# Kernel tuning notes

Measured on AMD Instinct MI355X. Metric: run time of the kernel, lower is better.

The kernel has to match this reference:

```python
import jax, jax.numpy as jnp
import numpy as np

GRID = (32, 32, 32)  # (W, H, D) from init_kwargs gridshape


def setup_inputs() -> dict:
    key = jax.random.key(0)
    k1, k2 = jax.random.split(key)
    N, F = 500000, 128
    features = jax.random.normal(k1, (N, F), dtype=jnp.float32)
    points = jax.random.uniform(k2, (N, 3), dtype=jnp.float32)  # locations in [0,1)^3
    return {"features": features, "points": points}


def reference(features, points):
    W, H, D = GRID
    # voxel index per point: floor(p * [W,H,D]), clipped into the grid
    dims = jnp.array([W, H, D], dtype=points.dtype)
    idx = jnp.floor(points * dims).astype(jnp.int32)
    idx = jnp.clip(idx, 0, jnp.array([W - 1, H - 1, D - 1], dtype=jnp.int32))
    cell = idx[:, 0] * (H * D) + idx[:, 1] * D + idx[:, 2]  # flat cell id [N]
    # scatter-max of point features into cells
    pooled = jax.ops.segment_max(features, cell, num_segments=W * H * D)
    # CUDA kernel initializes feat_cells to 0 (indices -1): empty cells and
    # cells whose max feature is negative stay at 0.
    return jnp.maximum(pooled, 0.0)
```

## Files before the change

### kernel.cpp

```cpp
#include <hip/hip_runtime.h>


constexpr int NCELL = 32 * 32 * 32;
constexpr int CAP   = 64;
constexpr int NF    = 128;

__global__ void bin_kernel(const float* __restrict__ points,
                           int* __restrict__ count,
                           int* __restrict__ bins, int n) {
    int i = blockIdx.x * blockDim.x + threadIdx.x;
    if (i >= n) return;
    float x = points[3 * i + 0] * 32.0f;
    float y = points[3 * i + 1] * 32.0f;
    float z = points[3 * i + 2] * 32.0f;
    int ix = (int)floorf(x); ix = ix < 0 ? 0 : (ix > 31 ? 31 : ix);
    int iy = (int)floorf(y); iy = iy < 0 ? 0 : (iy > 31 ? 31 : iy);
    int iz = (int)floorf(z); iz = iz < 0 ? 0 : (iz > 31 ? 31 : iz);
    int cell = (ix << 10) | (iy << 5) | iz;
    int slot = atomicAdd(&count[cell], 1);
    if (slot < CAP) bins[(cell << 6) + slot] = i;
}

__global__ __launch_bounds__(NF) void reduce_kernel(
        const float* __restrict__ feats,
        const int* __restrict__ count,
        const int* __restrict__ bins,
        float* __restrict__ out) {
    int cell = blockIdx.x;
    int t = threadIdx.x;
    int cnt = count[cell];
    if (cnt > CAP) cnt = CAP;
    const int* bp = bins + (cell << 6);

    float m = 0.0f;
    int k = 0;
    for (; k + 4 <= cnt; k += 4) {
        int p0 = bp[k], p1 = bp[k + 1], p2 = bp[k + 2], p3 = bp[k + 3];
        float a = feats[(size_t)p0 * NF + t];
        float b = feats[(size_t)p1 * NF + t];
        float c = feats[(size_t)p2 * NF + t];
        float d = feats[(size_t)p3 * NF + t];
        m = fmaxf(m, fmaxf(fmaxf(a, b), fmaxf(c, d)));
    }
    for (; k < cnt; k++)
        m = fmaxf(m, feats[(size_t)bp[k] * NF + t]);

    out[((size_t)cell << 7) + t] = m;
}

extern "C" void kernel_launch(void* const* d_in, const int* in_sizes, int n_in,
                              void* d_out, int out_size, void* d_ws, size_t ws_size,
                              hipStream_t stream) {
    const float* features = (const float*)d_in[0];
    const float* points   = (const float*)d_in[1];
    int n = in_sizes[1] / 3;

    int* bins  = (int*)d_ws;
    int* count = (int*)((char*)d_ws + (size_t)NCELL * CAP * 4);

    hipMemsetAsync(count, 0, NCELL * sizeof(int), stream);

    bin_kernel<<<(n + 255) / 256, 256, 0, stream>>>(points, count, bins, n);

    reduce_kernel<<<NCELL, NF, 0, stream>>>(
        features, count, bins, (float*)d_out);
}
```

Before: 383.9 us.

## Split cell reduction across four point groups with float4 loads

The reduce kernel now assigns 32 lanes per point, each loading a float4, so one block handles four points at once instead of walking them one after another. Bin indices are staged in shared memory, and the four partial maxima are combined through shared memory before a single float4 store. This gives more memory parallelism per block and wider loads, at the cost of two barriers and a final reduction step done by only 32 threads.

```diff
diff --git a/kernel.cpp b/kernel.cpp
--- a/kernel.cpp
+++ b/kernel.cpp
@@ -21,31 +21,50 @@
     if (slot < CAP) bins[(cell << 6) + slot] = i;
 }
 
-__global__ __launch_bounds__(NF) void reduce_kernel(
-        const float* __restrict__ feats,
+__device__ __forceinline__ float4 max4(float4 a, float4 b) {
+    float4 r;
+    r.x = fmaxf(a.x, b.x); r.y = fmaxf(a.y, b.y);
+    r.z = fmaxf(a.z, b.z); r.w = fmaxf(a.w, b.w);
+    return r;
+}
+
+__global__ __launch_bounds__(128) void reduce_kernel(
+        const float4* __restrict__ feats4,
         const int* __restrict__ count,
         const int* __restrict__ bins,
-        float* __restrict__ out) {
+        float4* __restrict__ out4) {
     int cell = blockIdx.x;
-    int t = threadIdx.x;
+    int tid  = threadIdx.x;
+    int lane = tid & 31;
+    int g    = tid >> 5;
+
+    __shared__ int    sbins[CAP];
+    __shared__ float4 part[4][32];
+
     int cnt = count[cell];
     if (cnt > CAP) cnt = CAP;
-    const int* bp = bins + (cell << 6);
+    if (tid < CAP) sbins[tid] = bins[(cell << 6) + tid];
+    __syncthreads();
 
-    float m = 0.0f;
-    int k = 0;
-    for (; k + 4 <= cnt; k += 4) {
-        int p0 = bp[k], p1 = bp[k + 1], p2 = bp[k + 2], p3 = bp[k + 3];
-        float a = feats[(size_t)p0 * NF + t];
-        float b = feats[(size_t)p1 * NF + t];
-        float c = feats[(size_t)p2 * NF + t];
-        float d = feats[(size_t)p3 * NF + t];
-        m = fmaxf(m, fmaxf(fmaxf(a, b), fmaxf(c, d)));
+    float4 m = make_float4(0.f, 0.f, 0.f, 0.f);
+    int k = g;
+    for (; k + 4 < cnt; k += 8) {
+        int p0 = sbins[k], p1 = sbins[k + 4];
+        float4 a = feats4[(size_t)p0 * 32 + lane];
+        float4 b = feats4[(size_t)p1 * 32 + lane];
+        m = max4(m, max4(a, b));
     }
-    for (; k < cnt; k++)
-        m = fmaxf(m, feats[(size_t)bp[k] * NF + t]);
+    if (k < cnt)
+        m = max4(m, feats4[(size_t)sbins[k] * 32 + lane]);
 
-    out[((size_t)cell << 7) + t] = m;
+    part[g][lane] = m;
+    __syncthreads();
+
+    if (tid < 32) {
+        float4 a = part[0][tid], b = part[1][tid];
+        float4 c = part[2][tid], d = part[3][tid];
+        out4[(size_t)cell * 32 + tid] = max4(max4(a, b), max4(c, d));
+    }
 }
 
 extern "C" void kernel_launch(void* const* d_in, const int* in_sizes, int n_in,
@@ -62,6 +81,6 @@
 
     bin_kernel<<<(n + 255) / 256, 256, 0, stream>>>(points, count, bins, n);
 
-    reduce_kernel<<<NCELL, NF, 0, stream>>>(
-        features, count, bins, (float*)d_out);
+    reduce_kernel<<<NCELL, 128, 0, stream>>>(
+        (const float4*)features, count, bins, (float4*)d_out);
 }
```

Result: no change. 382.2 us (-0.4%).

## Vectorize reduce kernel with float4 loads and one wave per cell

Applied to the files above, without the earlier changes.

Rewrites the reduce kernel so each 64-lane wave handles one cell. Each half-wave covers alternate point rows, loading features as float4 with nontemporal hints and merging the two halves with a cross-lane shuffle. Four cells are packed into each 256-thread block. The goal is more bytes per load instruction and more memory parallelism per wave on the gather-bound reduction. The cost is extra predication, out-of-range bin index reads past cnt (these stay within each cell's 64-slot bin), and a shuffle step.

```diff
diff --git a/kernel.cpp b/kernel.cpp
--- a/kernel.cpp
+++ b/kernel.cpp
@@ -3,7 +3,8 @@
 
 constexpr int NCELL = 32 * 32 * 32;
 constexpr int CAP   = 64;
-constexpr int NF    = 128;
+
+typedef float f4 __attribute__((ext_vector_type(4)));
 
 __global__ void bin_kernel(const float* __restrict__ points,
                            int* __restrict__ count,
@@ -21,31 +22,47 @@
     if (slot < CAP) bins[(cell << 6) + slot] = i;
 }
 
-__global__ __launch_bounds__(NF) void reduce_kernel(
-        const float* __restrict__ feats,
+__device__ __forceinline__ f4 max4(f4 a, f4 b) {
+    f4 r;
+    r.x = fmaxf(a.x, b.x); r.y = fmaxf(a.y, b.y);
+    r.z = fmaxf(a.z, b.z); r.w = fmaxf(a.w, b.w);
+    return r;
+}
+
+__global__ __launch_bounds__(256) void reduce_kernel(
+        const f4* __restrict__ feats4,
         const int* __restrict__ count,
         const int* __restrict__ bins,
-        float* __restrict__ out) {
-    int cell = blockIdx.x;
-    int t = threadIdx.x;
+        f4* __restrict__ out4) {
+    int wave = threadIdx.x >> 6;
+    int lane = threadIdx.x & 63;
+    int cell = (blockIdx.x << 2) + wave;
+    int sub  = lane >> 5;
+    int col  = lane & 31;
+
     int cnt = count[cell];
     if (cnt > CAP) cnt = CAP;
     const int* bp = bins + (cell << 6);
 
-    float m = 0.0f;
-    int k = 0;
-    for (; k + 4 <= cnt; k += 4) {
-        int p0 = bp[k], p1 = bp[k + 1], p2 = bp[k + 2], p3 = bp[k + 3];
-        float a = feats[(size_t)p0 * NF + t];
-        float b = feats[(size_t)p1 * NF + t];
-        float c = feats[(size_t)p2 * NF + t];
-        float d = feats[(size_t)p3 * NF + t];
-        m = fmaxf(m, fmaxf(fmaxf(a, b), fmaxf(c, d)));
+    const f4 zero = {0.f, 0.f, 0.f, 0.f};
+    f4 m = zero;
+    for (int k = 0; k < cnt; k += 8) {
+        int r0 = k + sub, r1 = k + 2 + sub, r2 = k + 4 + sub, r3 = k + 6 + sub;
+        int i0 = bp[r0], i1 = bp[r1], i2 = bp[r2], i3 = bp[r3];
+        f4 a = (r0 < cnt) ? __builtin_nontemporal_load(feats4 + (size_t)i0 * 32 + col) : zero;
+        f4 b = (r1 < cnt) ? __builtin_nontemporal_load(feats4 + (size_t)i1 * 32 + col) : zero;
+        f4 c = (r2 < cnt) ? __builtin_nontemporal_load(feats4 + (size_t)i2 * 32 + col) : zero;
+        f4 d = (r3 < cnt) ? __builtin_nontemporal_load(feats4 + (size_t)i3 * 32 + col) : zero;
+        m = max4(m, max4(max4(a, b), max4(c, d)));
     }
-    for (; k < cnt; k++)
-        m = fmaxf(m, feats[(size_t)bp[k] * NF + t]);
 
-    out[((size_t)cell << 7) + t] = m;
+    m.x = fmaxf(m.x, __shfl_xor(m.x, 32, 64));
+    m.y = fmaxf(m.y, __shfl_xor(m.y, 32, 64));
+    m.z = fmaxf(m.z, __shfl_xor(m.z, 32, 64));
+    m.w = fmaxf(m.w, __shfl_xor(m.w, 32, 64));
+
+    if (sub == 0)
+        __builtin_nontemporal_store(m, out4 + (size_t)cell * 32 + col);
 }
 
 extern "C" void kernel_launch(void* const* d_in, const int* in_sizes, int n_in,
@@ -62,6 +79,6 @@
 
     bin_kernel<<<(n + 255) / 256, 256, 0, stream>>>(points, count, bins, n);
 
-    reduce_kernel<<<NCELL, NF, 0, stream>>>(
-        features, count, bins, (float*)d_out);
+    reduce_kernel<<<NCELL / 4, 256, 0, stream>>>(
+        (const f4*)features, count, bins, (f4*)d_out);
 }
```

After: 359.9 us. -6.3%, faster.
